# Optimization experiments

Measured on AMD Instinct MI355X. Metric: run time of the kernel, lower is better.

Reference implementation:

```python
import jax, jax.numpy as jnp
import numpy as np

N_NODES = 100000
N_EDGES = 1600000
D_IN = 64
D_HID = 64
NEG_SLOPE = 0.01  # torch leaky_relu default


def _sage_conv(x, src, dst, W_l, b_l, W_r):
    # PyG SAGEConv (mean aggr): lin_l(mean_j x_j) + lin_r(x_i)
    n = x.shape[0]
    msg = x[src]  # [E, D] irregular gather
    agg = jax.ops.segment_sum(msg, dst, num_segments=n)
    deg = jax.ops.segment_sum(jnp.ones((src.shape[0],), x.dtype), dst, num_segments=n)
    mean = agg / jnp.maximum(deg, 1.0)[:, None]
    return mean @ W_l.T + b_l + x @ W_r.T


def setup_inputs() -> dict:
    key = jax.random.key(0)
    ks = jax.random.split(key, 12)
    x = jax.random.normal(ks[0], (N_NODES, D_IN), dtype=jnp.float32)
    edge_index = jax.random.randint(ks[1], (2, N_EDGES), 0, N_NODES, dtype=jnp.int64)
    s = 1.0 / np.sqrt(D_IN)
    params = {}
    dims = [(D_IN, D_HID), (D_HID, D_HID), (D_HID, D_HID)]
    ki = 2
    for i, (din, dout) in enumerate(dims, start=1):
        sc = 1.0 / np.sqrt(din)
        params[f'W_l{i}'] = jax.random.uniform(ks[ki], (dout, din), minval=-sc, maxval=sc, dtype=jnp.float32); ki += 1
        params[f'b_l{i}'] = jnp.zeros((dout,), jnp.float32)
        params[f'W_r{i}'] = jax.random.uniform(ks[ki], (dout, din), minval=-sc, maxval=sc, dtype=jnp.float32); ki += 1
    sc = 1.0 / np.sqrt(D_HID)
    params['W_out'] = jax.random.uniform(ks[ki], (1, D_HID), minval=-sc, maxval=sc, dtype=jnp.float32)
    params['b_out'] = jnp.zeros((1,), jnp.float32)
    return {'x': x, 'edge_index': edge_index, **params}


def reference(x, edge_index, W_l1, b_l1, W_r1, W_l2, b_l2, W_r2, W_l3, b_l3, W_r3, W_out, b_out):
    src, dst = edge_index[0], edge_index[1]
    h = x
    for (Wl, bl, Wr) in ((W_l1, b_l1, W_r1), (W_l2, b_l2, W_r2), (W_l3, b_l3, W_r3)):
        h = _sage_conv(h, src, dst, Wl, bl, Wr)
        h = jnp.where(h >= 0, h, NEG_SLOPE * h)
        # dropout is identity in eval mode
    return h @ W_out.T + b_out  # [N, 1]
```

## Files before the change

### kernel.cpp

```cpp
#include <hip/hip_runtime.h>
#include <hip/hip_fp16.h>

#define D 64
#define NEG_SLOPE 0.01f
#define CB_SHIFT 9
#define CB_NODES 512
#define MAXCB 256
#define CHUNK 8192
#define BCAP 10240
#define SADJ_CAP 10240
#define SA_STRIDE 132
#define SW_STRIDE 68

struct GemmSmem {
    float sA[64 * SA_STRIDE];
    float sW[64 * SW_STRIDE];
};
struct ScatSmem {
    int hist[MAXCB];
    int lofs[MAXCB];
    int gbase[MAXCB];
    int cur[MAXCB];
    int swsum[4];
    unsigned spk[CHUNK];
    unsigned char sbk[CHUNK];
};
union FusedSmem { GemmSmem g; ScatSmem s; };

__device__ __forceinline__ int detect64(const void* __restrict__ ei) {
    int lane = threadIdx.x & 63;
    int v = ((const int*)ei)[2 * lane + 1];
    return (__ballot(v != 0) == 0ULL) ? 1 : 0;
}

__device__ __forceinline__ int edge_at(const void* __restrict__ ei, long long idx, int is64) {
    if (is64) return (int)((const long long*)ei)[idx];
    return ((const int*)ei)[idx];
}

__device__ __forceinline__ void scatter_body(ScatSmem& sm,
        const void* __restrict__ ei, long long E,
        int* __restrict__ bcursor, unsigned* __restrict__ ebuf,
        int ncb, int bid) {
    int t = threadIdx.x;
    sm.hist[t] = 0;
    int is64 = detect64(ei);
    __syncthreads();
    long long start = (long long)bid * CHUNK;
    int ccnt = (int)min((long long)CHUNK, E - start);

    for (int i = t; i < ccnt; i += 256) {
        int d = edge_at(ei, E + start + i, is64);
        atomicAdd(&sm.hist[d >> CB_SHIFT], 1);
    }
    __syncthreads();
    {
        int v = sm.hist[t];
        int lane = t & 63, w = t >> 6;
        int inc = v;
        for (int off = 1; off < 64; off <<= 1) {
            int u = __shfl_up(inc, off, 64);
            if (lane >= off) inc += u;
        }
        if (lane == 63) sm.swsum[w] = inc;
        __syncthreads();
        int wof = 0;
        for (int i = 0; i < w; ++i) wof += sm.swsum[i];
        sm.lofs[t] = wof + inc - v;
    }
    if (t < ncb && sm.hist[t]) sm.gbase[t] = atomicAdd(&bcursor[t], sm.hist[t]);
    __syncthreads();
    sm.cur[t] = sm.lofs[t];
    __syncthreads();

    for (int i = t; i < ccnt; i += 256) {
        int s = edge_at(ei, start + i, is64);
        int d = edge_at(ei, E + start + i, is64);
        int b = d >> CB_SHIFT;
        int slot = atomicAdd(&sm.cur[b], 1);
        sm.spk[slot] = ((unsigned)s << CB_SHIFT) | (unsigned)(d & (CB_NODES - 1));
        sm.sbk[slot] = (unsigned char)b;
    }
    __syncthreads();

    for (int i = t; i < ccnt; i += 256) {
        int b = sm.sbk[i];
        int dst = sm.gbase[b] + (i - sm.lofs[b]);
        if (dst < BCAP) ebuf[(size_t)b * BCAP + dst] = sm.spk[i];
    }
}

__device__ __forceinline__ void stage_tile_T(float* __restrict__ sA,
        const float* __restrict__ g, int node_base, int N, int t) {
    int nq = t >> 4;
    int kq = t & 15;
#pragma unroll
    for (int p = 0; p < 8; ++p) {
        int node = p * 16 + nq;
        int gn = node_base + node;
        if (gn >= N) gn = N - 1;
        const float4 v = *(const float4*)(g + (size_t)gn * D + (kq << 2));
        sA[(kq * 4 + 0) * SA_STRIDE + node] = v.x;
        sA[(kq * 4 + 1) * SA_STRIDE + node] = v.y;
        sA[(kq * 4 + 2) * SA_STRIDE + node] = v.z;
        sA[(kq * 4 + 3) * SA_STRIDE + node] = v.w;
    }
}

__device__ __forceinline__ void stage_w_T(float* __restrict__ sW,
        const float* __restrict__ W, int t) {
    int cq = t >> 4;
    int kq = t & 15;
#pragma unroll
    for (int p = 0; p < 4; ++p) {
        int c = p * 16 + cq;
        const float4 v = *(const float4*)(W + c * D + (kq << 2));
        sW[(kq * 4 + 0) * SW_STRIDE + c] = v.x;
        sW[(kq * 4 + 1) * SW_STRIDE + c] = v.y;
        sW[(kq * 4 + 2) * SW_STRIDE + c] = v.z;
        sW[(kq * 4 + 3) * SW_STRIDE + c] = v.w;
    }
}

__device__ __forceinline__ void kloop4(float acc[8][4],
        const float* __restrict__ sA, const float* __restrict__ sW,
        int ng, int cg) {
#pragma unroll 4
    for (int k = 0; k < 64; ++k) {
        const float4 qa0 = *(const float4*)&sA[k * SA_STRIDE + ng * 8];
        const float4 qa1 = *(const float4*)&sA[k * SA_STRIDE + ng * 8 + 4];
        const float4 qb  = *(const float4*)&sW[k * SW_STRIDE + cg * 4];
        float av[8] = {qa0.x, qa0.y, qa0.z, qa0.w, qa1.x, qa1.y, qa1.z, qa1.w};
        float bv[4] = {qb.x, qb.y, qb.z, qb.w};
#pragma unroll
        for (int i = 0; i < 8; ++i)
#pragma unroll
            for (int j = 0; j < 4; ++j)
                acc[i][j] = __builtin_fmaf(av[i], bv[j], acc[i][j]);
    }
}

__device__ __forceinline__ void gemm_body(GemmSmem& sm,
        const float* __restrict__ h, const float* __restrict__ Wl,
        const float* __restrict__ Wr, const float* __restrict__ bl,
        __half* __restrict__ P, float* __restrict__ R, int N, int bid) {
    int t = threadIdx.x;
    int node_base = bid * 128;

    stage_tile_T(sm.sA, h, node_base, N, t);
    stage_w_T(sm.sW, Wl, t);
    __syncthreads();

    int ng = t >> 4;
    int cg = t & 15;
    float accP[8][4], accR[8][4];
#pragma unroll
    for (int i = 0; i < 8; ++i)
#pragma unroll
        for (int j = 0; j < 4; ++j) { accP[i][j] = 0.f; accR[i][j] = 0.f; }

    kloop4(accP, sm.sA, sm.sW, ng, cg);
    __syncthreads();
    stage_w_T(sm.sW, Wr, t);
    __syncthreads();
    kloop4(accR, sm.sA, sm.sW, ng, cg);

    const float4 bq = *(const float4*)&bl[cg * 4];
#pragma unroll
    for (int i = 0; i < 8; ++i) {
        int gn = node_base + ng * 8 + i;
        if (gn < N) {
            __half2* ph = (__half2*)(P + (size_t)gn * D + cg * 4);
            ph[0] = __floats2half2_rn(accP[i][0], accP[i][1]);
            ph[1] = __floats2half2_rn(accP[i][2], accP[i][3]);
            *(float4*)(R + (size_t)gn * D + cg * 4) =
                make_float4(accR[i][0] + bq.x, accR[i][1] + bq.y,
                            accR[i][2] + bq.z, accR[i][3] + bq.w);
        }
    }
}

__global__ __launch_bounds__(256, 3) void gemm1_scatter_kernel(
        const void* __restrict__ ei, long long E,
        int* __restrict__ bcursor, unsigned* __restrict__ ebuf, int ncb, int sgrid,
        const float* __restrict__ h, const float* __restrict__ Wl,
        const float* __restrict__ Wr, const float* __restrict__ bl,
        __half* __restrict__ P, float* __restrict__ R, int N) {
    __shared__ FusedSmem sm;
    if ((int)blockIdx.x < sgrid) {
        scatter_body(sm.s, ei, E, bcursor, ebuf, ncb, blockIdx.x);
    } else {
        gemm_body(sm.g, h, Wl, Wr, bl, P, R, N, blockIdx.x - sgrid);
    }
}

__global__ __launch_bounds__(256, 3) void gemm_kernel(
        const float* __restrict__ h, const float* __restrict__ Wl,
        const float* __restrict__ Wr, const float* __restrict__ bl,
        __half* __restrict__ P, float* __restrict__ R, int N) {
    __shared__ GemmSmem sm;
    gemm_body(sm, h, Wl, Wr, bl, P, R, N, blockIdx.x);
}

__global__ __launch_bounds__(256) void finefill_kernel(
        const unsigned* __restrict__ ebuf, const int* __restrict__ bcount,
        int* __restrict__ rowptr, int* __restrict__ adj, int N, int ncb) {
    __shared__ int cnt[CB_NODES];
    __shared__ int cur[CB_NODES];
    __shared__ int wpart[4];
    __shared__ int wsum4[4];
    __shared__ int se0;
    __shared__ int sAdj[SADJ_CAP];
    int t = threadIdx.x;
    int b = blockIdx.x;

    {
        int v = (t < ncb) ? min(bcount[t], BCAP) : 0;
        int lane = t & 63, w = t >> 6;
        int inc = v;
        for (int off = 1; off < 64; off <<= 1) {
            int u = __shfl_up(inc, off, 64);
            if (lane >= off) inc += u;
        }
        if (lane == 63) wsum4[w] = inc;
        __syncthreads();
        int wof = 0;
        for (int iw = 0; iw < w; ++iw) wof += wsum4[iw];
        int ex = wof + inc - v;
        if (t == b) se0 = ex;
        if (b == 0 && t == 0)
            rowptr[N] = wsum4[0] + wsum4[1] + wsum4[2] + wsum4[3];
    }
    __syncthreads();
    int e0 = se0;
    int len = min(bcount[b], BCAP);
    int nb = b << CB_SHIFT;
    const unsigned* slab = ebuf + (size_t)b * BCAP;

    cnt[2 * t] = 0; cnt[2 * t + 1] = 0;
    __syncthreads();
    for (int i = t; i < len; i += 256) {
        unsigned p = slab[i];
        atomicAdd(&cnt[p & (CB_NODES - 1)], 1);
    }
    __syncthreads();

    int c0 = cnt[2 * t], c1 = cnt[2 * t + 1];
    int s = c0 + c1;
    int lane = t & 63, wv = t >> 6;
    int inc = s;
    for (int off = 1; off < 64; off <<= 1) {
        int u = __shfl_up(inc, off, 64);
        if (lane >= off) inc += u;
    }
    if (lane == 63) wpart[wv] = inc;
    __syncthreads();
    int wof = 0;
    for (int w = 0; w < wv; ++w) wof += wpart[w];
    int ex = wof + inc - s;
    cur[2 * t] = ex; cur[2 * t + 1] = ex + c0;
    {
        int g = nb + 2 * t;
        if (g < N)     rowptr[g]     = e0 + ex;
        if (g + 1 < N) rowptr[g + 1] = e0 + ex + c0;
    }
    __syncthreads();

    int big = (len > SADJ_CAP);
    for (int i = t; i < len; i += 256) {
        unsigned p = slab[i];
        int dl = (int)(p & (CB_NODES - 1));
        int src = (int)(p >> CB_SHIFT);
        int pos = atomicAdd(&cur[dl], 1);
        if (big) adj[e0 + pos] = src;
        else     sAdj[pos] = src;
    }
    __syncthreads();
    if (!big) {
        for (int i = t; i < len; i += 256) adj[e0 + i] = sAdj[i];
    }
}

__global__ __launch_bounds__(256) void agg3_kernel(
        const __half* __restrict__ P, const float* __restrict__ R,
        const int* __restrict__ rowptr, const int* __restrict__ adj,
        const float* __restrict__ Wout, const float* __restrict__ bout,
        float* __restrict__ hout, float* __restrict__ out,
        int N, int final_flag) {
    int tid = blockIdx.x * blockDim.x + threadIdx.x;
    int i = tid >> 3;
    int sub = tid & 7;
    if (i >= N) return;

    int b0 = rowptr[i], b1 = rowptr[i + 1];
    float a0 = 0.f, a1 = 0.f, a2 = 0.f, a3 = 0.f;
    float a4 = 0.f, a5 = 0.f, a6 = 0.f, a7 = 0.f;
    size_t cofs = (size_t)(sub << 3);

    int e = b0;
    int nfull = (b1 - b0) >> 2;
#pragma unroll 2
    for (int q = 0; q < nfull; ++q) {
        int s0 = adj[e], s1 = adj[e + 1], s2 = adj[e + 2], s3 = adj[e + 3];
        e += 4;
        union { float4 f4; __half2 h2[4]; } u0, u1, u2, u3;
        u0.f4 = *(const float4*)(P + (size_t)s0 * D + cofs);
        u1.f4 = *(const float4*)(P + (size_t)s1 * D + cofs);
        u2.f4 = *(const float4*)(P + (size_t)s2 * D + cofs);
        u3.f4 = *(const float4*)(P + (size_t)s3 * D + cofs);
#define ACC8(u) { \
        float2 v0 = __half22float2(u.h2[0]); float2 v1 = __half22float2(u.h2[1]); \
        float2 v2 = __half22float2(u.h2[2]); float2 v3 = __half22float2(u.h2[3]); \
        a0 += v0.x; a1 += v0.y; a2 += v1.x; a3 += v1.y; \
        a4 += v2.x; a5 += v2.y; a6 += v3.x; a7 += v3.y; }
        ACC8(u0) ACC8(u1) ACC8(u2) ACC8(u3)
    }
    for (; e < b1; ++e) {
        int s = adj[e];
        union { float4 f4; __half2 h2[4]; } u;
        u.f4 = *(const float4*)(P + (size_t)s * D + cofs);
        ACC8(u)
    }
#undef ACC8

    float inv = 1.0f / fmaxf((float)(b1 - b0), 1.0f);
    const float4 r0 = *(const float4*)(R + (size_t)i * D + cofs);
    const float4 r1 = *(const float4*)(R + (size_t)i * D + cofs + 4);
    float y0 = a0 * inv + r0.x; y0 = (y0 >= 0.f) ? y0 : NEG_SLOPE * y0;
    float y1 = a1 * inv + r0.y; y1 = (y1 >= 0.f) ? y1 : NEG_SLOPE * y1;
    float y2 = a2 * inv + r0.z; y2 = (y2 >= 0.f) ? y2 : NEG_SLOPE * y2;
    float y3 = a3 * inv + r0.w; y3 = (y3 >= 0.f) ? y3 : NEG_SLOPE * y3;
    float y4 = a4 * inv + r1.x; y4 = (y4 >= 0.f) ? y4 : NEG_SLOPE * y4;
    float y5 = a5 * inv + r1.y; y5 = (y5 >= 0.f) ? y5 : NEG_SLOPE * y5;
    float y6 = a6 * inv + r1.z; y6 = (y6 >= 0.f) ? y6 : NEG_SLOPE * y6;
    float y7 = a7 * inv + r1.w; y7 = (y7 >= 0.f) ? y7 : NEG_SLOPE * y7;
    if (!final_flag) {
        *(float4*)(hout + (size_t)i * D + cofs) = make_float4(y0, y1, y2, y3);
        *(float4*)(hout + (size_t)i * D + cofs + 4) = make_float4(y4, y5, y6, y7);
    } else {
        const float4 w0 = *(const float4*)(Wout + cofs);
        const float4 w1 = *(const float4*)(Wout + cofs + 4);
        float p = y0 * w0.x + y1 * w0.y + y2 * w0.z + y3 * w0.w
                + y4 * w1.x + y5 * w1.y + y6 * w1.z + y7 * w1.w;
        p += __shfl_xor(p, 1, 64);
        p += __shfl_xor(p, 2, 64);
        p += __shfl_xor(p, 4, 64);
        if (sub == 0) out[i] = p + bout[0];
    }
}

extern "C" void kernel_launch(void* const* d_in, const int* in_sizes, int n_in,
                              void* d_out, int out_size, void* d_ws, size_t ws_size,
                              hipStream_t stream) {
    const float* x    = (const float*)d_in[0];
    const void*  ei   = d_in[1];
    const float* Wl1  = (const float*)d_in[2];
    const float* bl1  = (const float*)d_in[3];
    const float* Wr1  = (const float*)d_in[4];
    const float* Wl2  = (const float*)d_in[5];
    const float* bl2  = (const float*)d_in[6];
    const float* Wr2  = (const float*)d_in[7];
    const float* Wl3  = (const float*)d_in[8];
    const float* bl3  = (const float*)d_in[9];
    const float* Wr3  = (const float*)d_in[10];
    const float* Wout = (const float*)d_in[11];
    const float* bout = (const float*)d_in[12];
    float* out = (float*)d_out;

    int       N = in_sizes[0] / D;
    long long E = (long long)in_sizes[1] / 2;
    int ncb = (N + CB_NODES - 1) >> CB_SHIFT;

    char* ws = (char*)d_ws;
    size_t off = 256;
    int* bcursor = (int*)(ws + off); off += 1024;
    int* rowptr = (int*)(ws + off); off += (((size_t)(N + 1) * 4 + 255) / 256) * 256;
    int* adj    = (int*)(ws + off); off += (((size_t)E * 4 + 255) / 256) * 256;
    unsigned* ebuf = (unsigned*)(ws + off); off += (size_t)ncb * BCAP * 4;
    float* B1 = (float*)(ws + off); off += (size_t)N * D * 4;
    __half* B2h = (__half*)(ws + off);

    int sgrid = (int)((E + CHUNK - 1) / CHUNK);
    int ggrid = (N + 127) / 128;
    int agrid = (N * 8 + 255) / 256;

    hipMemsetAsync(bcursor, 0, 1024, stream);

    gemm1_scatter_kernel<<<sgrid + ggrid, 256, 0, stream>>>(
        ei, E, bcursor, ebuf, ncb, sgrid,
        x, Wl1, Wr1, bl1, B2h, B1, N);
    finefill_kernel<<<ncb, 256, 0, stream>>>(ebuf, bcursor, rowptr, adj, N, ncb);
    agg3_kernel<<<agrid, 256, 0, stream>>>(B2h, B1, rowptr, adj, Wout, bout, B1, out, N, 0);
    gemm_kernel<<<ggrid, 256, 0, stream>>>(B1, Wl2, Wr2, bl2, B2h, B1, N);
    agg3_kernel<<<agrid, 256, 0, stream>>>(B2h, B1, rowptr, adj, Wout, bout, B1, out, N, 0);
    gemm_kernel<<<ggrid, 256, 0, stream>>>(B1, Wl3, Wr3, bl3, B2h, B1, N);
    agg3_kernel<<<agrid, 256, 0, stream>>>(B2h, B1, rowptr, adj, Wout, bout, B1, out, N, 1);
}
```

Measured before the change: 310.7 us.

## Fuse Wl/Wr GEMM passes with half-precision weights and split finefill blocks

The GEMM now stages Wl and Wr together as fp16 in shared memory and computes both accumulators in a single k-loop. This removes the second weight staging and its barriers and halves weight LDS traffic, at the cost of weight precision and higher register pressure. The finefill kernel now launches two blocks per coarse bucket, each handling half of the 512 destination nodes, so there is more parallelism and less shared memory per block. In exchange, each block re-reads the whole slab to count and filter its half.

```diff
diff --git a/kernel.cpp b/kernel.cpp
--- a/kernel.cpp
+++ b/kernel.cpp
@@ -8,13 +8,13 @@
 #define MAXCB 256
 #define CHUNK 8192
 #define BCAP 10240
-#define SADJ_CAP 10240
+#define HCAP 6144
 #define SA_STRIDE 132
-#define SW_STRIDE 68
+#define SWH_STRIDE 136
 
 struct GemmSmem {
-    float sA[64 * SA_STRIDE];
-    float sW[64 * SW_STRIDE];
+    float  sA[64 * SA_STRIDE];
+    __half sW[64 * SWH_STRIDE];
 };
 struct ScatSmem {
     int hist[MAXCB];
@@ -107,36 +107,23 @@
     }
 }
 
-__device__ __forceinline__ void stage_w_T(float* __restrict__ sW,
-        const float* __restrict__ W, int t) {
+__device__ __forceinline__ void stage_wlr_h(__half* __restrict__ sW,
+        const float* __restrict__ Wl, const float* __restrict__ Wr, int t) {
     int cq = t >> 4;
     int kq = t & 15;
 #pragma unroll
-    for (int p = 0; p < 4; ++p) {
-        int c = p * 16 + cq;
-        const float4 v = *(const float4*)(W + c * D + (kq << 2));
-        sW[(kq * 4 + 0) * SW_STRIDE + c] = v.x;
-        sW[(kq * 4 + 1) * SW_STRIDE + c] = v.y;
-        sW[(kq * 4 + 2) * SW_STRIDE + c] = v.z;
-        sW[(kq * 4 + 3) * SW_STRIDE + c] = v.w;
-    }
-}
-
-__device__ __forceinline__ void kloop4(float acc[8][4],
-        const float* __restrict__ sA, const float* __restrict__ sW,
-        int ng, int cg) {
-#pragma unroll 4
-    for (int k = 0; k < 64; ++k) {
-        const float4 qa0 = *(const float4*)&sA[k * SA_STRIDE + ng * 8];
-        const float4 qa1 = *(const float4*)&sA[k * SA_STRIDE + ng * 8 + 4];
-        const float4 qb  = *(const float4*)&sW[k * SW_STRIDE + cg * 4];
-        float av[8] = {qa0.x, qa0.y, qa0.z, qa0.w, qa1.x, qa1.y, qa1.z, qa1.w};
-        float bv[4] = {qb.x, qb.y, qb.z, qb.w};
-#pragma unroll
-        for (int i = 0; i < 8; ++i)
-#pragma unroll
-            for (int j = 0; j < 4; ++j)
-                acc[i][j] = __builtin_fmaf(av[i], bv[j], acc[i][j]);
+    for (int j = 0; j < 4; ++j) {
+        int c = cq * 4 + j;
+        const float4 vl = *(const float4*)(Wl + c * D + (kq << 2));
+        const float4 vr = *(const float4*)(Wr + c * D + (kq << 2));
+        sW[(kq * 4 + 0) * SWH_STRIDE + cq * 8 + j]     = __float2half(vl.x);
+        sW[(kq * 4 + 1) * SWH_STRIDE + cq * 8 + j]     = __float2half(vl.y);
+        sW[(kq * 4 + 2) * SWH_STRIDE + cq * 8 + j]     = __float2half(vl.z);
+        sW[(kq * 4 + 3) * SWH_STRIDE + cq * 8 + j]     = __float2half(vl.w);
+        sW[(kq * 4 + 0) * SWH_STRIDE + cq * 8 + 4 + j] = __float2half(vr.x);
+        sW[(kq * 4 + 1) * SWH_STRIDE + cq * 8 + 4 + j] = __float2half(vr.y);
+        sW[(kq * 4 + 2) * SWH_STRIDE + cq * 8 + 4 + j] = __float2half(vr.z);
+        sW[(kq * 4 + 3) * SWH_STRIDE + cq * 8 + 4 + j] = __float2half(vr.w);
     }
 }
 
@@ -148,7 +135,7 @@
     int node_base = bid * 128;
 
     stage_tile_T(sm.sA, h, node_base, N, t);
-    stage_w_T(sm.sW, Wl, t);
+    stage_wlr_h(sm.sW, Wl, Wr, t);
     __syncthreads();
 
     int ng = t >> 4;
@@ -159,11 +146,28 @@
 #pragma unroll
         for (int j = 0; j < 4; ++j) { accP[i][j] = 0.f; accR[i][j] = 0.f; }
 
-    kloop4(accP, sm.sA, sm.sW, ng, cg);
-    __syncthreads();
-    stage_w_T(sm.sW, Wr, t);
-    __syncthreads();
-    kloop4(accR, sm.sA, sm.sW, ng, cg);
+#pragma unroll 2
+    for (int k = 0; k < 64; ++k) {
+        const float4 qa0 = *(const float4*)&sm.sA[k * SA_STRIDE + ng * 8];
+        const float4 qa1 = *(const float4*)&sm.sA[k * SA_STRIDE + ng * 8 + 4];
+        union { float4 f4; __half2 h2[4]; } uw;
+        uw.f4 = *(const float4*)&sm.sW[k * SWH_STRIDE + cg * 8];
+        float2 l01 = __half22float2(uw.h2[0]);
+        float2 l23 = __half22float2(uw.h2[1]);
+        float2 r01 = __half22float2(uw.h2[2]);
+        float2 r23 = __half22float2(uw.h2[3]);
+        float av[8] = {qa0.x, qa0.y, qa0.z, qa0.w, qa1.x, qa1.y, qa1.z, qa1.w};
+        float wl[4] = {l01.x, l01.y, l23.x, l23.y};
+        float wr[4] = {r01.x, r01.y, r23.x, r23.y};
+#pragma unroll
+        for (int i = 0; i < 8; ++i) {
+#pragma unroll
+            for (int j = 0; j < 4; ++j) {
+                accP[i][j] = __builtin_fmaf(av[i], wl[j], accP[i][j]);
+                accR[i][j] = __builtin_fmaf(av[i], wr[j], accR[i][j]);
+            }
+        }
+    }
 
     const float4 bq = *(const float4*)&bl[cg * 4];
 #pragma unroll
@@ -205,14 +209,15 @@
 __global__ __launch_bounds__(256) void finefill_kernel(
         const unsigned* __restrict__ ebuf, const int* __restrict__ bcount,
         int* __restrict__ rowptr, int* __restrict__ adj, int N, int ncb) {
-    __shared__ int cnt[CB_NODES];
-    __shared__ int cur[CB_NODES];
+    __shared__ int cnt[256];
+    __shared__ int cur[256];
     __shared__ int wpart[4];
     __shared__ int wsum4[4];
-    __shared__ int se0;
-    __shared__ int sAdj[SADJ_CAP];
+    __shared__ int se0, sbelow;
+    __shared__ int sAdj[HCAP];
     int t = threadIdx.x;
-    int b = blockIdx.x;
+    int b = blockIdx.x >> 1;
+    int half = blockIdx.x & 1;
 
     {
         int v = (t < ncb) ? min(bcount[t], BCAP) : 0;
@@ -223,32 +228,40 @@
             if (lane >= off) inc += u;
         }
         if (lane == 63) wsum4[w] = inc;
+        if (t == 0) sbelow = 0;
         __syncthreads();
         int wof = 0;
         for (int iw = 0; iw < w; ++iw) wof += wsum4[iw];
         int ex = wof + inc - v;
         if (t == b) se0 = ex;
-        if (b == 0 && t == 0)
+        if (blockIdx.x == 0 && t == 0)
             rowptr[N] = wsum4[0] + wsum4[1] + wsum4[2] + wsum4[3];
     }
     __syncthreads();
-    int e0 = se0;
+    int e0b = se0;
     int len = min(bcount[b], BCAP);
-    int nb = b << CB_SHIFT;
     const unsigned* slab = ebuf + (size_t)b * BCAP;
 
-    cnt[2 * t] = 0; cnt[2 * t + 1] = 0;
-    __syncthreads();
+    cnt[t] = 0;
+    __syncthreads();
+    int below = 0;
     for (int i = t; i < len; i += 256) {
-        unsigned p = slab[i];
-        atomicAdd(&cnt[p & (CB_NODES - 1)], 1);
-    }
-    __syncthreads();
-
-    int c0 = cnt[2 * t], c1 = cnt[2 * t + 1];
-    int s = c0 + c1;
+        int dl = (int)(slab[i] & (CB_NODES - 1));
+        below += (dl < 256) ? 1 : 0;
+        if ((dl >> 8) == half) atomicAdd(&cnt[dl & 255], 1);
+    }
+#pragma unroll
+    for (int off = 32; off > 0; off >>= 1) below += __shfl_xor(below, off, 64);
+    if ((t & 63) == 0) atomicAdd(&sbelow, below);
+    __syncthreads();
+
+    int e0 = e0b + (half ? sbelow : 0);
+    int hlen = half ? (len - sbelow) : sbelow;
+    int nb = (b << CB_SHIFT) + (half << 8);
+
+    int v = cnt[t];
     int lane = t & 63, wv = t >> 6;
-    int inc = s;
+    int inc = v;
     for (int off = 1; off < 64; off <<= 1) {
         int u = __shfl_up(inc, off, 64);
         if (lane >= off) inc += u;
@@ -257,27 +270,27 @@
     __syncthreads();
     int wof = 0;
     for (int w = 0; w < wv; ++w) wof += wpart[w];
-    int ex = wof + inc - s;
-    cur[2 * t] = ex; cur[2 * t + 1] = ex + c0;
+    int ex = wof + inc - v;
+    cur[t] = ex;
     {
-        int g = nb + 2 * t;
-        if (g < N)     rowptr[g]     = e0 + ex;
-        if (g + 1 < N) rowptr[g + 1] = e0 + ex + c0;
-    }
-    __syncthreads();
-
-    int big = (len > SADJ_CAP);
+        int g = nb + t;
+        if (g < N) rowptr[g] = e0 + ex;
+    }
+    __syncthreads();
+
+    int big = (hlen > HCAP);
     for (int i = t; i < len; i += 256) {
         unsigned p = slab[i];
         int dl = (int)(p & (CB_NODES - 1));
+        if ((dl >> 8) != half) continue;
         int src = (int)(p >> CB_SHIFT);
-        int pos = atomicAdd(&cur[dl], 1);
+        int pos = atomicAdd(&cur[dl & 255], 1);
         if (big) adj[e0 + pos] = src;
         else     sAdj[pos] = src;
     }
     __syncthreads();
     if (!big) {
-        for (int i = t; i < len; i += 256) adj[e0 + i] = sAdj[i];
+        for (int i = t; i < hlen; i += 256) adj[e0 + i] = sAdj[i];
     }
 }
 
@@ -389,7 +402,7 @@
     gemm1_scatter_kernel<<<sgrid + ggrid, 256, 0, stream>>>(
         ei, E, bcursor, ebuf, ncb, sgrid,
         x, Wl1, Wr1, bl1, B2h, B1, N);
-    finefill_kernel<<<ncb, 256, 0, stream>>>(ebuf, bcursor, rowptr, adj, N, ncb);
+    finefill_kernel<<<ncb * 2, 256, 0, stream>>>(ebuf, bcursor, rowptr, adj, N, ncb);
     agg3_kernel<<<agrid, 256, 0, stream>>>(B2h, B1, rowptr, adj, Wout, bout, B1, out, N, 0);
     gemm_kernel<<<ggrid, 256, 0, stream>>>(B1, Wl2, Wr2, bl2, B2h, B1, N);
     agg3_kernel<<<agrid, 256, 0, stream>>>(B2h, B1, rowptr, adj, Wout, bout, B1, out, N, 0);
```

After: 314.4 us. No clear change (+1.2%).
